# Kernel tuning notes

Hardware: AMD Instinct MI355X
Metric: run time of the kernel (lower is better)

## Reference

```python
import jax, jax.numpy as jnp
import numpy as np


def setup_inputs() -> dict:
    key = jax.random.key(0)
    k1, k2, k3, k4 = jax.random.split(key, 4)
    B, T, E, H, D = 4, 2048, 1024, 16, 64
    x = jax.random.normal(k1, (B, T, E), dtype=jnp.float32)
    # wv stored as [E, H*D] so y = x @ wv (math-equivalent to nn.Linear weight.T)
    wv = jax.random.normal(k2, (E, H * D), dtype=jnp.float32) * (1.0 / E) ** 0.5
    wr = jax.random.normal(k3, (H, E, T), dtype=jnp.float32) * (2.0 / E) ** 0.5
    wo = jax.random.normal(k4, (H * D, E), dtype=jnp.float32) * (1.0 / (H * D)) ** 0.5
    return {"x": x, "wv": wv, "wr": wr, "wo": wo}


def reference(x, wv, wr, wo):
    B, T, E = x.shape
    H = wr.shape[0]
    HD = wv.shape[1]
    D = HD // H
    # values: [B, H, T, D]
    v = (x @ wv).reshape(B, T, H, D).transpose(0, 2, 1, 3)
    # per-key scores, identical for every query row: s[b,h,k]
    s = jnp.einsum('bte,het->bht', x, wr[:, :, :T]) / jnp.sqrt(jnp.asarray(D, x.dtype))
    # causal softmax over keys k<=q with scores shared across queries reduces to
    # a prefix-softmax-weighted cumulative sum over V (exact same math, O(T)):
    # out[q] = sum_{k<=q} exp(s_k - m) v_k / sum_{k<=q} exp(s_k - m)
    m = jnp.max(s, axis=-1, keepdims=True)          # global max is a valid stable shift
    e = jnp.exp(s - m)                              # [B,H,T]
    num = jnp.cumsum(e[..., None] * v, axis=2)      # [B,H,T,D]
    den = jnp.cumsum(e, axis=2)[..., None]          # [B,H,T,1]
    out = num / den                                 # [B,H,T,D]
    out = out.transpose(0, 2, 1, 3).reshape(B, T, HD)
    return out @ wo
```

## Files before the change

kernel.cpp:

```cpp
#include <hip/hip_runtime.h>
#include <stdint.h>

typedef unsigned short u16;
typedef __attribute__((ext_vector_type(8))) short short8;
typedef __attribute__((ext_vector_type(4))) float f32x4;

#define B_  4
#define T_  2048
#define E_  1024
#define H_  16
#define D_  64
#define HD_ 1024
#define BT_ (B_*T_)
#define TC_ 64
#define NC_ (T_/TC_)
#define SG_ 32
#define SEB_ (E_/SG_)
#define SHB_ 4

__device__ __forceinline__ u16 f2b(float f) {
  uint32_t u = __float_as_uint(f);
  uint32_t r = (u + 0x7FFFu + ((u >> 16) & 1u)) >> 16;
  return (u16)r;
}
__device__ __forceinline__ float b2f(u16 u) {
  return __uint_as_float(((uint32_t)u) << 16);
}

__global__ __launch_bounds__(256) void prep_x(const float* __restrict__ x,
                                              u16* __restrict__ xb,
                                              u16* __restrict__ xTb) {
  __shared__ float tile[64][65];
  const int b = blockIdx.x, t0 = blockIdx.y * 64, e0 = blockIdx.z * 64;
  const int c4 = (threadIdx.x & 15) * 4;
  const int rw = threadIdx.x >> 4;
#pragma unroll
  for (int r = 0; r < 4; ++r) {
    const int row = r * 16 + rw;
    const float4 v4 = *reinterpret_cast<const float4*>(
        &x[((size_t)b * T_ + t0 + row) * E_ + e0 + c4]);
    tile[row][c4 + 0] = v4.x; tile[row][c4 + 1] = v4.y;
    tile[row][c4 + 2] = v4.z; tile[row][c4 + 3] = v4.w;
    ushort4 o;
    o.x = f2b(v4.x); o.y = f2b(v4.y); o.z = f2b(v4.z); o.w = f2b(v4.w);
    *reinterpret_cast<ushort4*>(&xb[((size_t)(b * T_ + t0 + row)) * E_ + e0 + c4]) = o;
  }
  __syncthreads();
#pragma unroll
  for (int r = 0; r < 4; ++r) {
    const int erow = r * 16 + rw;
    ushort4 o;
    o.x = f2b(tile[c4 + 0][erow]);
    o.y = f2b(tile[c4 + 1][erow]);
    o.z = f2b(tile[c4 + 2][erow]);
    o.w = f2b(tile[c4 + 3][erow]);
    *reinterpret_cast<ushort4*>(&xTb[((size_t)b * E_ + e0 + erow) * T_ + t0 + c4]) = o;
  }
}

__global__ __launch_bounds__(256) void transpose_w2(const float* __restrict__ wv,
                                                    const float* __restrict__ wo,
                                                    u16* __restrict__ wvT,
                                                    u16* __restrict__ woT) {
  __shared__ float tile[64][65];
  const float* in = blockIdx.z ? wo : wv;
  u16* out = blockIdx.z ? woT : wvT;
  const int r0 = blockIdx.x * 64, c0 = blockIdx.y * 64;
  const int tx = threadIdx.x & 63, ty = threadIdx.x >> 6;
#pragma unroll
  for (int r = 0; r < 16; ++r) {
    int row = r * 4 + ty;
    tile[row][tx] = in[(size_t)(r0 + row) * 1024 + c0 + tx];
  }
  __syncthreads();
#pragma unroll
  for (int r = 0; r < 16; ++r) {
    int row = r * 4 + ty;
    out[(size_t)(c0 + row) * 1024 + r0 + tx] = f2b(tile[tx][row]);
  }
}

template <int OUT_BF16>
__global__ __launch_bounds__(256) void gemm_bt(const u16* __restrict__ A,
                                               const u16* __restrict__ Bt,
                                               float* __restrict__ Cf,
                                               u16* __restrict__ Cb,
                                               int M, int N, int K) {
  __shared__ __align__(16) u16 As[128 * 64];
  __shared__ __align__(16) u16 Bs[128 * 64];
  const int tid  = threadIdx.x;
  const int lane = tid & 63;
  const int wave = tid >> 6;
  const int wr_  = wave >> 1, wc_ = wave & 1;

  const int nwg = gridDim.x * gridDim.y;
  const int bid = blockIdx.y * gridDim.x + blockIdx.x;
  const int cpx = nwg >> 3;
  const int swz = (bid & 7) * cpx + (bid >> 3);
  const int bx = swz % gridDim.x, by = swz / gridDim.x;
  const int brow = by * 128;
  const int bcol = bx * 128;
  const int l15 = lane & 15, l4 = lane >> 4;

  f32x4 acc[4][4];
  const f32x4 zero = {0.f, 0.f, 0.f, 0.f};
#pragma unroll
  for (int i = 0; i < 4; ++i)
#pragma unroll
    for (int j = 0; j < 4; ++j) acc[i][j] = zero;

  for (int k0 = 0; k0 < K; k0 += 64) {
#pragma unroll
    for (int s2 = 0; s2 < 4; ++s2) {
      const int c = s2 * 256 + tid;
      const int row = c >> 3, g = c & 7;
      const u16* ga = A  + (size_t)(brow + row) * K + k0 + g * 8;
      const u16* gb = Bt + (size_t)(bcol + row) * K + k0 + g * 8;
      u16* la = &As[(size_t)(s2 * 256 + wave * 64) * 8];
      u16* lb = &Bs[(size_t)(s2 * 256 + wave * 64) * 8];
      __builtin_amdgcn_global_load_lds((const __attribute__((address_space(1))) void*)ga,
                                       (__attribute__((address_space(3))) void*)la,
                                       16, 0, 0);
      __builtin_amdgcn_global_load_lds((const __attribute__((address_space(1))) void*)gb,
                                       (__attribute__((address_space(3))) void*)lb,
                                       16, 0, 0);
    }
    __syncthreads();

    short8 af[2][4], bfr[2][4];
#pragma unroll
    for (int kk = 0; kk < 2; ++kk) {
#pragma unroll
      for (int mi = 0; mi < 4; ++mi)
        af[kk][mi] = *reinterpret_cast<const short8*>(
            &As[(wr_ * 64 + mi * 16 + l15) * 64 + kk * 32 + l4 * 8]);
#pragma unroll
      for (int ni = 0; ni < 4; ++ni)
        bfr[kk][ni] = *reinterpret_cast<const short8*>(
            &Bs[(wc_ * 64 + ni * 16 + l15) * 64 + kk * 32 + l4 * 8]);
    }
#pragma unroll
    for (int kk = 0; kk < 2; ++kk)
#pragma unroll
      for (int mi = 0; mi < 4; ++mi)
#pragma unroll
        for (int ni = 0; ni < 4; ++ni)
          acc[mi][ni] = __builtin_amdgcn_mfma_f32_16x16x32_bf16(af[kk][mi], bfr[kk][ni],
                                                                acc[mi][ni], 0, 0, 0);
    __syncthreads();
  }

#pragma unroll
  for (int mi = 0; mi < 4; ++mi) {
#pragma unroll
    for (int ni = 0; ni < 4; ++ni) {
      const int col = bcol + wc_ * 64 + ni * 16 + l15;
#pragma unroll
      for (int j = 0; j < 4; ++j) {
        const int row = brow + wr_ * 64 + mi * 16 + l4 * 4 + j;
        if (OUT_BF16) Cb[(size_t)row * N + col] = f2b(acc[mi][ni][j]);
        else          Cf[(size_t)row * N + col] = acc[mi][ni][j];
      }
    }
  }
}

__global__ __launch_bounds__(256) void score_partial(const u16* __restrict__ xTb,
                                                     const float* __restrict__ wr,
                                                     float* __restrict__ partial) {
  const int t  = blockIdx.x * 256 + threadIdx.x;
  const int g  = blockIdx.y;
  const int e0 = g * SEB_;
  const int h0 = blockIdx.z * SHB_;
  float acc[4][SHB_];
#pragma unroll
  for (int b = 0; b < 4; ++b)
#pragma unroll
    for (int hh = 0; hh < SHB_; ++hh) acc[b][hh] = 0.f;

#pragma unroll 4
  for (int ee = 0; ee < SEB_; ++ee) {
    const int e = e0 + ee;
    float xv[4];
#pragma unroll
    for (int b = 0; b < 4; ++b) xv[b] = b2f(xTb[((size_t)b * E_ + e) * T_ + t]);
#pragma unroll
    for (int hh = 0; hh < SHB_; ++hh) {
      float w = wr[((size_t)(h0 + hh) * E_ + e) * T_ + t];
#pragma unroll
      for (int b = 0; b < 4; ++b) acc[b][hh] = fmaf(xv[b], w, acc[b][hh]);
    }
  }
  float* pp = partial + (size_t)g * (B_ * H_ * T_);
#pragma unroll
  for (int b = 0; b < 4; ++b)
#pragma unroll
    for (int hh = 0; hh < SHB_; ++hh)
      pp[((size_t)b * H_ + h0 + hh) * T_ + t] = acc[b][hh] * 0.125f;
}

__global__ __launch_bounds__(256) void score_reduce(const float* __restrict__ partial,
                                                    float* __restrict__ s) {
  const int i = blockIdx.x * 256 + threadIdx.x;
  float a = 0.f;
#pragma unroll
  for (int g = 0; g < SG_; ++g) a += partial[(size_t)g * (B_ * H_ * T_) + i];
  s[i] = a;
}

__global__ __launch_bounds__(256) void chunk_sums(const float* __restrict__ s,
                                                  const u16* __restrict__ v,
                                                  float* __restrict__ sev,
                                                  float* __restrict__ se,
                                                  float* __restrict__ mc) {
  const int bh = blockIdx.y;
  const int b = bh >> 4, h = bh & 15;
  const int w = threadIdx.x >> 6, d = threadIdx.x & 63;
  const int c = blockIdx.x * 4 + w;
  const float* sp = s + (size_t)bh * T_ + c * TC_;

  float lm = sp[d];
#pragma unroll
  for (int off = 1; off < 64; off <<= 1) lm = fmaxf(lm, __shfl_xor(lm, off, 64));

  const u16* vp = v + ((size_t)(b * T_ + c * TC_)) * HD_ + h * D_ + d;
  float acc = 0.f, ae = 0.f;
#pragma unroll 8
  for (int tt = 0; tt < TC_; ++tt) {
    float e = __expf(sp[tt] - lm);
    acc = fmaf(e, b2f(vp[(size_t)tt * HD_]), acc);
    ae += e;
  }
  sev[((size_t)bh * NC_ + c) * D_ + d] = acc;
  if (d == 0) { se[bh * NC_ + c] = ae; mc[bh * NC_ + c] = lm; }
}

__global__ __launch_bounds__(256) void chunk_scan(const float* __restrict__ s,
                                                  const u16* __restrict__ v,
                                                  const float* __restrict__ sev,
                                                  const float* __restrict__ se,
                                                  const float* __restrict__ mc,
                                                  u16* __restrict__ attn) {
  const int bh = blockIdx.y;
  const int b = bh >> 4, h = bh & 15;
  const int w = threadIdx.x >> 6, d = threadIdx.x & 63;
  const int c = blockIdx.x * 4 + w;
  const float* mcp = mc + bh * NC_;

  float gm = (d < NC_) ? mcp[d] : -1e30f;
#pragma unroll
  for (int off = 1; off < 64; off <<= 1) gm = fmaxf(gm, __shfl_xor(gm, off, 64));

  const float* sevp = sev + (size_t)bh * NC_ * D_;
  const float* sep  = se + bh * NC_;
  float pn = 0.f, pd = 0.f;
  for (int c2 = 0; c2 < c; ++c2) {
    float f = __expf(mcp[c2] - gm);
    pn = fmaf(sevp[(size_t)c2 * D_ + d], f, pn);
    pd = fmaf(sep[c2], f, pd);
  }

  const float* sp = s + (size_t)bh * T_ + c * TC_;
  const u16* vp = v + ((size_t)(b * T_ + c * TC_)) * HD_ + h * D_ + d;
  u16* ap = attn + ((size_t)(b * T_ + c * TC_)) * HD_ + h * D_ + d;
#pragma unroll 8
  for (int tt = 0; tt < TC_; ++tt) {
    float e = __expf(sp[tt] - gm);
    pn = fmaf(e, b2f(vp[(size_t)tt * HD_]), pn);
    pd += e;
    ap[(size_t)tt * HD_] = f2b(__fdividef(pn, pd));
  }
}

extern "C" void kernel_launch(void* const* d_in, const int* in_sizes, int n_in,
                              void* d_out, int out_size, void* d_ws, size_t ws_size,
                              hipStream_t stream) {
  const float* x  = (const float*)d_in[0];
  const float* wv = (const float*)d_in[1];
  const float* wr = (const float*)d_in[2];
  const float* wo = (const float*)d_in[3];
  float* out = (float*)d_out;

  char* ws = (char*)d_ws;
  size_t off = 0;
  auto alloc = [&](size_t bytes) {
    void* p = ws + off;
    off += (bytes + 255) & ~(size_t)255;
    return p;
  };
  u16*   xb   = (u16*)  alloc((size_t)BT_ * E_ * 2);
  u16*   xTb  = (u16*)  alloc((size_t)B_ * E_ * T_ * 2);
  u16*   wvT  = (u16*)  alloc((size_t)HD_ * E_ * 2);
  u16*   woT  = (u16*)  alloc((size_t)E_ * HD_ * 2);
  u16*   vv   = (u16*)  alloc((size_t)BT_ * HD_ * 2);
  u16*   attn = (u16*)  alloc((size_t)BT_ * HD_ * 2);
  float* s    = (float*)alloc((size_t)B_ * H_ * T_ * 4);
  float* sev  = (float*)alloc((size_t)B_ * H_ * NC_ * D_ * 4);
  float* se   = (float*)alloc((size_t)B_ * H_ * NC_ * 4);
  float* mc   = (float*)alloc((size_t)B_ * H_ * NC_ * 4);
  float* part = (float*)alloc((size_t)SG_ * B_ * H_ * T_ * 4);

  prep_x<<<dim3(B_, T_ / 64, E_ / 64), 256, 0, stream>>>(x, xb, xTb);
  transpose_w2<<<dim3(16, 16, 2), 256, 0, stream>>>(wv, wo, wvT, woT);

  gemm_bt<1><<<dim3(HD_ / 128, BT_ / 128), 256, 0, stream>>>(xb, wvT, nullptr, vv, BT_, HD_, E_);

  score_partial<<<dim3(T_ / 256, SG_, H_ / SHB_), 256, 0, stream>>>(xTb, wr, part);
  score_reduce<<<(B_ * H_ * T_) / 256, 256, 0, stream>>>(part, s);

  chunk_sums<<<dim3(NC_ / 4, B_ * H_), 256, 0, stream>>>(s, vv, sev, se, mc);
  chunk_scan<<<dim3(NC_ / 4, B_ * H_), 256, 0, stream>>>(s, vv, sev, se, mc, attn);

  gemm_bt<0><<<dim3(E_ / 128, BT_ / 128), 256, 0, stream>>>(attn, woT, out, nullptr, BT_, E_, HD_);
}
```

Before: 139.8 us.

## Pipeline GEMM with 4-slot LDS ring, 128x256 tiles and 8 waves

Rewrites the bf16 GEMM to use a 128x256 output tile with 512 threads (8 waves). It also stages K in 32-wide halves into a 4-slot LDS ring buffer with three stages prefetched, so global-to-LDS loads overlap with MFMA compute. Each step is synchronized by a single barrier with explicit vmcnt waits and raises wave priority around the MFMA block. The goal is to hide load latency and cut the per-iteration double barrier. In exchange it uses more LDS per block (96 KB), which lowers occupancy, and halves the grid size. The loop bound is hardcoded to 32 halves, which assumes K=1024.

```diff
diff --git a/kernel.cpp b/kernel.cpp
--- a/kernel.cpp
+++ b/kernel.cpp
@@ -81,17 +81,18 @@
 }
 
 template <int OUT_BF16>
-__global__ __launch_bounds__(256) void gemm_bt(const u16* __restrict__ A,
+__global__ __launch_bounds__(512) void gemm_bt(const u16* __restrict__ A,
                                                const u16* __restrict__ Bt,
                                                float* __restrict__ Cf,
                                                u16* __restrict__ Cb,
                                                int M, int N, int K) {
-  __shared__ __align__(16) u16 As[128 * 64];
-  __shared__ __align__(16) u16 Bs[128 * 64];
+  __shared__ __align__(16) u16 As[4][128 * 32];
+  __shared__ __align__(16) u16 Bs[4][256 * 32];
   const int tid  = threadIdx.x;
   const int lane = tid & 63;
   const int wave = tid >> 6;
-  const int wr_  = wave >> 1, wc_ = wave & 1;
+  const int wr_  = wave >> 2;
+  const int wc_  = wave & 3;
 
   const int nwg = gridDim.x * gridDim.y;
   const int bid = blockIdx.y * gridDim.x + blockIdx.x;
@@ -99,8 +100,10 @@
   const int swz = (bid & 7) * cpx + (bid >> 3);
   const int bx = swz % gridDim.x, by = swz / gridDim.x;
   const int brow = by * 128;
-  const int bcol = bx * 128;
+  const int bcol = bx * 256;
   const int l15 = lane & 15, l4 = lane >> 4;
+
+  const int NHALF = K / 32;
 
   f32x4 acc[4][4];
   const f32x4 zero = {0.f, 0.f, 0.f, 0.f};
@@ -109,46 +112,65 @@
 #pragma unroll
     for (int j = 0; j < 4; ++j) acc[i][j] = zero;
 
-  for (int k0 = 0; k0 < K; k0 += 64) {
-#pragma unroll
-    for (int s2 = 0; s2 < 4; ++s2) {
-      const int c = s2 * 256 + tid;
-      const int row = c >> 3, g = c & 7;
-      const u16* ga = A  + (size_t)(brow + row) * K + k0 + g * 8;
-      const u16* gb = Bt + (size_t)(bcol + row) * K + k0 + g * 8;
-      u16* la = &As[(size_t)(s2 * 256 + wave * 64) * 8];
-      u16* lb = &Bs[(size_t)(s2 * 256 + wave * 64) * 8];
-      __builtin_amdgcn_global_load_lds((const __attribute__((address_space(1))) void*)ga,
-                                       (__attribute__((address_space(3))) void*)la,
-                                       16, 0, 0);
-      __builtin_amdgcn_global_load_lds((const __attribute__((address_space(1))) void*)gb,
-                                       (__attribute__((address_space(3))) void*)lb,
-                                       16, 0, 0);
+  auto stage_half = [&](int hs) {
+    const int slot = hs & 3;
+    const int kof = hs * 32;
+    {
+      const int row = tid >> 2, g = tid & 3;
+      const u16* ga = A + (size_t)(brow + row) * K + kof + g * 8;
+      __builtin_amdgcn_global_load_lds(
+          (const __attribute__((address_space(1))) void*)ga,
+          (__attribute__((address_space(3))) void*)&As[slot][tid * 8], 16, 0, 0);
     }
-    __syncthreads();
-
-    short8 af[2][4], bfr[2][4];
-#pragma unroll
-    for (int kk = 0; kk < 2; ++kk) {
-#pragma unroll
-      for (int mi = 0; mi < 4; ++mi)
-        af[kk][mi] = *reinterpret_cast<const short8*>(
-            &As[(wr_ * 64 + mi * 16 + l15) * 64 + kk * 32 + l4 * 8]);
-#pragma unroll
-      for (int ni = 0; ni < 4; ++ni)
-        bfr[kk][ni] = *reinterpret_cast<const short8*>(
-            &Bs[(wc_ * 64 + ni * 16 + l15) * 64 + kk * 32 + l4 * 8]);
+#pragma unroll
+    for (int s2 = 0; s2 < 2; ++s2) {
+      const int c = s2 * 512 + tid;
+      const int row = c >> 2, g = c & 3;
+      const u16* gb = Bt + (size_t)(bcol + row) * K + kof + g * 8;
+      __builtin_amdgcn_global_load_lds(
+          (const __attribute__((address_space(1))) void*)gb,
+          (__attribute__((address_space(3))) void*)&Bs[slot][c * 8], 16, 0, 0);
     }
-#pragma unroll
-    for (int kk = 0; kk < 2; ++kk)
-#pragma unroll
-      for (int mi = 0; mi < 4; ++mi)
-#pragma unroll
-        for (int ni = 0; ni < 4; ++ni)
-          acc[mi][ni] = __builtin_amdgcn_mfma_f32_16x16x32_bf16(af[kk][mi], bfr[kk][ni],
-                                                                acc[mi][ni], 0, 0, 0);
-    __syncthreads();
-  }
+  };
+
+#define GPHASE(HS, VMCLIT, DOSTAGE)                                           \
+  do {                                                                        \
+    asm volatile("s_waitcnt vmcnt(" #VMCLIT ")" ::: "memory");                \
+    __builtin_amdgcn_s_barrier();                                             \
+    __builtin_amdgcn_sched_barrier(0);                                        \
+    if (DOSTAGE) stage_half((HS) + 3);                                        \
+    const int slot_ = (HS) & 3;                                               \
+    short8 af[4], bf[4];                                                      \
+    _Pragma("unroll")                                                         \
+    for (int mi = 0; mi < 4; ++mi)                                            \
+      af[mi] = *reinterpret_cast<const short8*>(                              \
+          &As[slot_][(wr_ * 64 + mi * 16 + l15) * 32 + l4 * 8]);              \
+    _Pragma("unroll")                                                         \
+    for (int ni = 0; ni < 4; ++ni)                                            \
+      bf[ni] = *reinterpret_cast<const short8*>(                              \
+          &Bs[slot_][(wc_ * 64 + ni * 16 + l15) * 32 + l4 * 8]);              \
+    asm volatile("s_waitcnt lgkmcnt(0)" ::: "memory");                        \
+    __builtin_amdgcn_sched_barrier(0);                                        \
+    __builtin_amdgcn_s_setprio(1);                                            \
+    _Pragma("unroll")                                                         \
+    for (int mi = 0; mi < 4; ++mi)                                            \
+      _Pragma("unroll")                                                       \
+      for (int ni = 0; ni < 4; ++ni)                                          \
+        acc[mi][ni] = __builtin_amdgcn_mfma_f32_16x16x32_bf16(                \
+            af[mi], bf[ni], acc[mi][ni], 0, 0, 0);                            \
+    __builtin_amdgcn_s_setprio(0);                                            \
+  } while (0)
+
+  stage_half(0);
+  stage_half(1);
+  stage_half(2);
+
+  for (int hs = 0; hs < 30; ++hs) {
+    GPHASE(hs, 6, hs < NHALF - 3);
+  }
+  GPHASE(30, 3, false);
+  GPHASE(31, 0, false);
+#undef GPHASE
 
 #pragma unroll
   for (int mi = 0; mi < 4; ++mi) {
@@ -303,7 +325,7 @@
   prep_x<<<dim3(B_, T_ / 64, E_ / 64), 256, 0, stream>>>(x, xb, xTb);
   transpose_w2<<<dim3(16, 16, 2), 256, 0, stream>>>(wv, wo, wvT, woT);
 
-  gemm_bt<1><<<dim3(HD_ / 128, BT_ / 128), 256, 0, stream>>>(xb, wvT, nullptr, vv, BT_, HD_, E_);
+  gemm_bt<1><<<dim3(HD_ / 256, BT_ / 128), 512, 0, stream>>>(xb, wvT, nullptr, vv, BT_, HD_, E_);
 
   score_partial<<<dim3(T_ / 256, SG_, H_ / SHB_), 256, 0, stream>>>(xTb, wr, part);
   score_reduce<<<(B_ * H_ * T_) / 256, 256, 0, stream>>>(part, s);
@@ -311,5 +333,5 @@
   chunk_sums<<<dim3(NC_ / 4, B_ * H_), 256, 0, stream>>>(s, vv, sev, se, mc);
   chunk_scan<<<dim3(NC_ / 4, B_ * H_), 256, 0, stream>>>(s, vv, sev, se, mc, attn);
 
-  gemm_bt<0><<<dim3(E_ / 128, BT_ / 128), 256, 0, stream>>>(attn, woT, out, nullptr, BT_, E_, HD_);
-}
+  gemm_bt<0><<<dim3(E_ / 256, BT_ / 128), 512, 0, stream>>>(attn, woT, out, nullptr, BT_, E_, HD_);
+}
```

Measured after the change: 144.9 us. 3.6% more time.

## Fuse prep kernels, interleave xT layout, bf16 score partials, fold reduce into chunk_sums

Applied to the files above, without the earlier changes.

Merges the x prep and weight transposes into one launch. Stores the transposed x with 8 e-values per t contiguous, so score_partial can do 16-byte vector loads, and halves the heads per block to get more blocks. Score partials are stored as bf16 and the separate reduce kernel is removed: chunk_sums now sums the 32 partials itself and keeps the chunk's scores in shared memory. Rounding the partials to bf16 adds error to the scores. Re-reading wr across more head-blocks may also cost some reuse.

```diff
diff --git a/kernel.cpp b/kernel.cpp
--- a/kernel.cpp
+++ b/kernel.cpp
@@ -3,6 +3,7 @@
 
 typedef unsigned short u16;
 typedef __attribute__((ext_vector_type(8))) short short8;
+typedef __attribute__((ext_vector_type(8))) unsigned short ushort8v;
 typedef __attribute__((ext_vector_type(4))) float f32x4;
 
 #define B_  4
@@ -16,7 +17,7 @@
 #define NC_ (T_/TC_)
 #define SG_ 32
 #define SEB_ (E_/SG_)
-#define SHB_ 4
+#define SHB_ 2
 
 __device__ __forceinline__ u16 f2b(float f) {
   uint32_t u = __float_as_uint(f);
@@ -27,56 +28,60 @@
   return __uint_as_float(((uint32_t)u) << 16);
 }
 
-__global__ __launch_bounds__(256) void prep_x(const float* __restrict__ x,
-                                              u16* __restrict__ xb,
-                                              u16* __restrict__ xTb) {
+__global__ __launch_bounds__(256) void prep_all(const float* __restrict__ x,
+                                                const float* __restrict__ wv,
+                                                const float* __restrict__ wo,
+                                                u16* __restrict__ xb,
+                                                u16* __restrict__ xTb8,
+                                                u16* __restrict__ wvT,
+                                                u16* __restrict__ woT) {
   __shared__ float tile[64][65];
-  const int b = blockIdx.x, t0 = blockIdx.y * 64, e0 = blockIdx.z * 64;
-  const int c4 = (threadIdx.x & 15) * 4;
-  const int rw = threadIdx.x >> 4;
-#pragma unroll
-  for (int r = 0; r < 4; ++r) {
-    const int row = r * 16 + rw;
-    const float4 v4 = *reinterpret_cast<const float4*>(
-        &x[((size_t)b * T_ + t0 + row) * E_ + e0 + c4]);
-    tile[row][c4 + 0] = v4.x; tile[row][c4 + 1] = v4.y;
-    tile[row][c4 + 2] = v4.z; tile[row][c4 + 3] = v4.w;
-    ushort4 o;
-    o.x = f2b(v4.x); o.y = f2b(v4.y); o.z = f2b(v4.z); o.w = f2b(v4.w);
-    *reinterpret_cast<ushort4*>(&xb[((size_t)(b * T_ + t0 + row)) * E_ + e0 + c4]) = o;
-  }
-  __syncthreads();
-#pragma unroll
-  for (int r = 0; r < 4; ++r) {
-    const int erow = r * 16 + rw;
-    ushort4 o;
-    o.x = f2b(tile[c4 + 0][erow]);
-    o.y = f2b(tile[c4 + 1][erow]);
-    o.z = f2b(tile[c4 + 2][erow]);
-    o.w = f2b(tile[c4 + 3][erow]);
-    *reinterpret_cast<ushort4*>(&xTb[((size_t)b * E_ + e0 + erow) * T_ + t0 + c4]) = o;
-  }
-}
-
-__global__ __launch_bounds__(256) void transpose_w2(const float* __restrict__ wv,
-                                                    const float* __restrict__ wo,
-                                                    u16* __restrict__ wvT,
-                                                    u16* __restrict__ woT) {
-  __shared__ float tile[64][65];
-  const float* in = blockIdx.z ? wo : wv;
-  u16* out = blockIdx.z ? woT : wvT;
-  const int r0 = blockIdx.x * 64, c0 = blockIdx.y * 64;
-  const int tx = threadIdx.x & 63, ty = threadIdx.x >> 6;
-#pragma unroll
-  for (int r = 0; r < 16; ++r) {
-    int row = r * 4 + ty;
-    tile[row][tx] = in[(size_t)(r0 + row) * 1024 + c0 + tx];
-  }
-  __syncthreads();
-#pragma unroll
-  for (int r = 0; r < 16; ++r) {
-    int row = r * 4 + ty;
-    out[(size_t)(c0 + row) * 1024 + r0 + tx] = f2b(tile[tx][row]);
+  const int bid = blockIdx.x;
+  if (bid < 2048) {
+    const int b = bid >> 9, rest = bid & 511;
+    const int t0 = (rest >> 4) * 64, e0 = (rest & 15) * 64;
+    const int c4 = (threadIdx.x & 15) * 4;
+    const int rw = threadIdx.x >> 4;
+#pragma unroll
+    for (int r = 0; r < 4; ++r) {
+      const int row = r * 16 + rw;
+      const float4 v4 = *reinterpret_cast<const float4*>(
+          &x[((size_t)b * T_ + t0 + row) * E_ + e0 + c4]);
+      tile[row][c4 + 0] = v4.x; tile[row][c4 + 1] = v4.y;
+      tile[row][c4 + 2] = v4.z; tile[row][c4 + 3] = v4.w;
+      ushort4 o;
+      o.x = f2b(v4.x); o.y = f2b(v4.y); o.z = f2b(v4.z); o.w = f2b(v4.w);
+      *reinterpret_cast<ushort4*>(&xb[((size_t)(b * T_ + t0 + row)) * E_ + e0 + c4]) = o;
+    }
+    __syncthreads();
+    const int tl = threadIdx.x & 63;
+    const int eg = threadIdx.x >> 6;
+#pragma unroll
+    for (int p = 0; p < 2; ++p) {
+      const int egg = eg + p * 4;
+      ushort8v o;
+#pragma unroll
+      for (int j = 0; j < 8; ++j) o[j] = f2b(tile[tl][egg * 8 + j]);
+      *reinterpret_cast<ushort8v*>(
+          &xTb8[((size_t)(b * (E_ / 8) + (e0 >> 3) + egg) * T_ + t0 + tl) * 8]) = o;
+    }
+  } else {
+    const int k = bid - 2048;
+    const float* in = (k >> 8) ? wo : wv;
+    u16* out = (k >> 8) ? woT : wvT;
+    const int r0 = ((k >> 4) & 15) * 64, c0 = (k & 15) * 64;
+    const int tx = threadIdx.x & 63, ty = threadIdx.x >> 6;
+#pragma unroll
+    for (int r = 0; r < 16; ++r) {
+      int row = r * 4 + ty;
+      tile[row][tx] = in[(size_t)(r0 + row) * 1024 + c0 + tx];
+    }
+    __syncthreads();
+#pragma unroll
+    for (int r = 0; r < 16; ++r) {
+      int row = r * 4 + ty;
+      out[(size_t)(c0 + row) * 1024 + r0 + tx] = f2b(tile[tx][row]);
+    }
   }
 }
 
@@ -165,12 +170,11 @@
   }
 }
 
-__global__ __launch_bounds__(256) void score_partial(const u16* __restrict__ xTb,
+__global__ __launch_bounds__(256) void score_partial(const u16* __restrict__ xTb8,
                                                      const float* __restrict__ wr,
-                                                     float* __restrict__ partial) {
+                                                     u16* __restrict__ partial) {
   const int t  = blockIdx.x * 256 + threadIdx.x;
   const int g  = blockIdx.y;
-  const int e0 = g * SEB_;
   const int h0 = blockIdx.z * SHB_;
   float acc[4][SHB_];
 #pragma unroll
@@ -178,38 +182,39 @@
 #pragma unroll
     for (int hh = 0; hh < SHB_; ++hh) acc[b][hh] = 0.f;
 
-#pragma unroll 4
-  for (int ee = 0; ee < SEB_; ++ee) {
-    const int e = e0 + ee;
-    float xv[4];
-#pragma unroll
-    for (int b = 0; b < 4; ++b) xv[b] = b2f(xTb[((size_t)b * E_ + e) * T_ + t]);
-#pragma unroll
-    for (int hh = 0; hh < SHB_; ++hh) {
-      float w = wr[((size_t)(h0 + hh) * E_ + e) * T_ + t];
-#pragma unroll
-      for (int b = 0; b < 4; ++b) acc[b][hh] = fmaf(xv[b], w, acc[b][hh]);
-    }
-  }
-  float* pp = partial + (size_t)g * (B_ * H_ * T_);
+#pragma unroll
+  for (int e8 = 0; e8 < SEB_ / 8; ++e8) {
+    const int eb = g * (SEB_ / 8) + e8;
+    ushort8v xv[4];
+#pragma unroll
+    for (int b = 0; b < 4; ++b)
+      xv[b] = *reinterpret_cast<const ushort8v*>(
+          &xTb8[((size_t)(b * (E_ / 8) + eb) * T_ + t) * 8]);
+#pragma unroll
+    for (int j = 0; j < 8; ++j) {
+      const int e = eb * 8 + j;
+      float xf[4];
+#pragma unroll
+      for (int b = 0; b < 4; ++b) xf[b] = b2f(xv[b][j]);
+#pragma unroll
+      for (int hh = 0; hh < SHB_; ++hh) {
+        const float w = wr[((size_t)(h0 + hh) * E_ + e) * T_ + t];
+#pragma unroll
+        for (int b = 0; b < 4; ++b) acc[b][hh] = fmaf(xf[b], w, acc[b][hh]);
+      }
+    }
+  }
+  u16* pp = partial + (size_t)g * (B_ * H_ * T_);
 #pragma unroll
   for (int b = 0; b < 4; ++b)
 #pragma unroll
     for (int hh = 0; hh < SHB_; ++hh)
-      pp[((size_t)b * H_ + h0 + hh) * T_ + t] = acc[b][hh] * 0.125f;
-}
-
-__global__ __launch_bounds__(256) void score_reduce(const float* __restrict__ partial,
-                                                    float* __restrict__ s) {
-  const int i = blockIdx.x * 256 + threadIdx.x;
-  float a = 0.f;
-#pragma unroll
-  for (int g = 0; g < SG_; ++g) a += partial[(size_t)g * (B_ * H_ * T_) + i];
-  s[i] = a;
-}
-
-__global__ __launch_bounds__(256) void chunk_sums(const float* __restrict__ s,
+      pp[((size_t)b * H_ + h0 + hh) * T_ + t] = f2b(acc[b][hh] * 0.125f);
+}
+
+__global__ __launch_bounds__(256) void chunk_sums(const u16* __restrict__ partial,
                                                   const u16* __restrict__ v,
+                                                  float* __restrict__ s,
                                                   float* __restrict__ sev,
                                                   float* __restrict__ se,
                                                   float* __restrict__ mc) {
@@ -217,9 +222,18 @@
   const int b = bh >> 4, h = bh & 15;
   const int w = threadIdx.x >> 6, d = threadIdx.x & 63;
   const int c = blockIdx.x * 4 + w;
-  const float* sp = s + (size_t)bh * T_ + c * TC_;
-
-  float lm = sp[d];
+  const int t = blockIdx.x * 256 + threadIdx.x;
+
+  float sv = 0.f;
+#pragma unroll
+  for (int g = 0; g < SG_; ++g)
+    sv += b2f(partial[(size_t)g * (B_ * H_ * T_) + (size_t)bh * T_ + t]);
+  s[(size_t)bh * T_ + t] = sv;
+
+  __shared__ float es[4][64];
+  es[w][d] = sv;
+
+  float lm = sv;
 #pragma unroll
   for (int off = 1; off < 64; off <<= 1) lm = fmaxf(lm, __shfl_xor(lm, off, 64));
 
@@ -227,7 +241,7 @@
   float acc = 0.f, ae = 0.f;
 #pragma unroll 8
   for (int tt = 0; tt < TC_; ++tt) {
-    float e = __expf(sp[tt] - lm);
+    float e = __expf(es[w][tt] - lm);
     acc = fmaf(e, b2f(vp[(size_t)tt * HD_]), acc);
     ae += e;
   }
@@ -289,7 +303,7 @@
     return p;
   };
   u16*   xb   = (u16*)  alloc((size_t)BT_ * E_ * 2);
-  u16*   xTb  = (u16*)  alloc((size_t)B_ * E_ * T_ * 2);
+  u16*   xTb8 = (u16*)  alloc((size_t)B_ * E_ * T_ * 2);
   u16*   wvT  = (u16*)  alloc((size_t)HD_ * E_ * 2);
   u16*   woT  = (u16*)  alloc((size_t)E_ * HD_ * 2);
   u16*   vv   = (u16*)  alloc((size_t)BT_ * HD_ * 2);
@@ -298,17 +312,15 @@
   float* sev  = (float*)alloc((size_t)B_ * H_ * NC_ * D_ * 4);
   float* se   = (float*)alloc((size_t)B_ * H_ * NC_ * 4);
   float* mc   = (float*)alloc((size_t)B_ * H_ * NC_ * 4);
-  float* part = (float*)alloc((size_t)SG_ * B_ * H_ * T_ * 4);
-
-  prep_x<<<dim3(B_, T_ / 64, E_ / 64), 256, 0, stream>>>(x, xb, xTb);
-  transpose_w2<<<dim3(16, 16, 2), 256, 0, stream>>>(wv, wo, wvT, woT);
+  u16*   part = (u16*)  alloc((size_t)SG_ * B_ * H_ * T_ * 2);
+
+  prep_all<<<2560, 256, 0, stream>>>(x, wv, wo, xb, xTb8, wvT, woT);
 
   gemm_bt<1><<<dim3(HD_ / 128, BT_ / 128), 256, 0, stream>>>(xb, wvT, nullptr, vv, BT_, HD_, E_);
 
-  score_partial<<<dim3(T_ / 256, SG_, H_ / SHB_), 256, 0, stream>>>(xTb, wr, part);
-  score_reduce<<<(B_ * H_ * T_) / 256, 256, 0, stream>>>(part, s);
-
-  chunk_sums<<<dim3(NC_ / 4, B_ * H_), 256, 0, stream>>>(s, vv, sev, se, mc);
+  score_partial<<<dim3(T_ / 256, SG_, H_ / SHB_), 256, 0, stream>>>(xTb8, wr, part);
+
+  chunk_sums<<<dim3(NC_ / 4, B_ * H_), 256, 0, stream>>>(part, vv, s, sev, se, mc);
   chunk_scan<<<dim3(NC_ / 4, B_ * H_), 256, 0, stream>>>(s, vv, sev, se, mc, attn);
 
   gemm_bt<0><<<dim3(E_ / 128, BT_ / 128), 256, 0, stream>>>(attn, woT, out, nullptr, BT_, E_, HD_);
```

Measured after the change: 130.3 us. 1.07x faster.
